# Kernel tuning notes

Hardware: AMD Instinct MI355X
Metric: run time of the kernel (lower is better)

Reference implementation:

```python
import jax, jax.numpy as jnp
import numpy as np

N, NFEAT, NFEAT_EXT, NHID, NCLASS, NHEADS = 8192, 512, 128, 256, 10, 8


def setup_inputs() -> dict:
    key = jax.random.key(0)
    ks = jax.random.split(key, 12)
    s = lambda fan_in: 1.0 / np.sqrt(fan_in)
    return {
        "x": jax.random.normal(ks[0], (N, NFEAT), jnp.float32),
        "adj": jax.random.uniform(ks[1], (N, N), jnp.float32) / N,  # row-stochastic-ish normalized adjacency
        "sub_fea": jax.random.normal(ks[2], (1, NFEAT_EXT), jnp.float32),
        # GraphConvolution 1: nfeat -> nhid
        "gc1_W": jax.random.normal(ks[3], (NFEAT, NHID), jnp.float32) * s(NFEAT),
        "gc1_b": jnp.zeros((NHID,), jnp.float32),
        # GraphConvolution 2: nhid -> 2*nhid
        "gc2_W": jax.random.normal(ks[4], (NHID, 2 * NHID), jnp.float32) * s(NHID),
        "gc2_b": jnp.zeros((2 * NHID,), jnp.float32),
        # fc1: nfeat_ext -> nhid
        "fc1_W": jax.random.normal(ks[5], (NFEAT_EXT, NHID), jnp.float32) * s(NFEAT_EXT),
        "fc1_b": jnp.zeros((NHID,), jnp.float32),
        # AttentionLayer(3*nhid, nclass, nheads): per-head projection + softmax head gating
        "att_W": jax.random.normal(ks[6], (NHEADS, 3 * NHID, NCLASS), jnp.float32) * s(3 * NHID),
        "att_a": jax.random.normal(ks[7], (NHEADS, 3 * NHID), jnp.float32) * s(3 * NHID),
        "att_b": jnp.zeros((NCLASS,), jnp.float32),
    }


def reference(x, adj, sub_fea, gc1_W, gc1_b, gc2_W, gc2_b, fc1_W, fc1_b, att_W, att_a, att_b):
    # GCN layer 1: adj @ (x @ W) + b, then ReLU
    h = jax.nn.relu(adj @ (x @ gc1_W) + gc1_b)            # [N, nhid]
    # GCN layer 2
    h = jax.nn.relu(adj @ (h @ gc2_W) + gc2_b)            # [N, 2*nhid]
    # global_mean_pool(batch=None): mean over all nodes -> single graph vector
    g = jax.nn.selu(jnp.mean(h, axis=0, keepdims=True))    # [1, 2*nhid]
    # dropout is identity in eval mode
    x_ext = sub_fea @ fc1_W + fc1_b                        # [1, nhid]
    z = jnp.concatenate([g, x_ext], axis=1)                # [1, 3*nhid]
    # multi-head attention fusion: softmax over head scores gating per-head projections
    scores = jnp.einsum("bi,hi->bh", z, att_a)            # [1, nheads]
    alpha = jax.nn.softmax(scores, axis=1)
    head_out = jnp.einsum("bi,hio->bho", z, att_W)        # [1, nheads, nclass]
    out = jnp.einsum("bh,bho->bo", alpha, head_out) + att_b  # [1, nclass]
    return jax.nn.log_softmax(out, axis=1)
```

## Files before the change

kernel.cpp:

```cpp
#include <hip/hip_runtime.h>

typedef __attribute__((ext_vector_type(8))) short short8;
typedef __attribute__((ext_vector_type(4))) float floatx4;
typedef unsigned short ushort_t;
typedef unsigned int u32;

__device__ __forceinline__ ushort_t f2bf(float x) {
  union { float f; unsigned int u; } v; v.f = x;
  unsigned int u = v.u;
  return (ushort_t)((u + 0x7FFFu + ((u >> 16) & 1u)) >> 16);
}
__device__ __forceinline__ unsigned int pk2(float a, float b) {
  return (unsigned int)f2bf(a) | ((unsigned int)f2bf(b) << 16);
}
__device__ __forceinline__ void gl_lds16(const void* g, void* l) {
  __builtin_amdgcn_global_load_lds(
      (const __attribute__((address_space(1))) u32*)g,
      (__attribute__((address_space(3))) u32*)l, 16, 0, 0);
}


__global__ void prep_t(const float* __restrict__ W1, const float* __restrict__ W2,
                       ushort_t* __restrict__ W1T, ushort_t* __restrict__ W2T) {
  int idx = blockIdx.x * 256 + threadIdx.x;
  int m = idx >> 9, k = idx & 511;
  W1T[((m >> 7) * 64 + (k >> 3)) * 1024 + (m & 127) * 8 + (k & 7)] = f2bf(W1[k * 256 + m]);
  int m2 = idx >> 8, k2 = idx & 255;
  W2T[((m2 >> 7) * 32 + (k2 >> 3)) * 1024 + (m2 & 127) * 8 + (k2 & 7)] = f2bf(W2[k2 * 512 + m2]);
}

__global__ __launch_bounds__(256) void tile_cvt(const float* __restrict__ src,
                                                ushort_t* __restrict__ dst, const int K) {
  __shared__ __align__(16) ushort_t ls[33024];
  const int t = threadIdx.x;
  const int rb = blockIdx.y, cb = blockIdx.x;
  const long sbase = (long)rb * 128 * K + cb * 256;
#pragma unroll 4
  for (int i = 0; i < 32; ++i) {
    int flat = i * 256 + t;
    int row = flat >> 6, kq = flat & 63;
    float4 v = *(const float4*)(src + sbase + (long)row * K + kq * 4);
    *(uint2*)(ls + ((kq >> 1) * 129 + row) * 8 + (kq & 1) * 4) =
        make_uint2(pk2(v.x, v.y), pk2(v.z, v.w));
  }
  __syncthreads();
  ushort_t* ob = dst + ((long)rb * (K >> 3) + cb * 32) * 1024;
  const uint4* lv = (const uint4*)ls;
  uint4* ov = (uint4*)ob;
#pragma unroll 4
  for (int i = 0; i < 16; ++i) {
    int o = i * 256 + t;
    ov[o] = lv[(o >> 7) * 129 + (o & 127)];
  }
}

template<int MT, int NT, int EPI>
__global__ __launch_bounds__(256, 2)
void gemm_t(const ushort_t* __restrict__ A, const ushort_t* __restrict__ B,
            const float* __restrict__ bias, float* __restrict__ Cf,
            float* __restrict__ gacc, const int K, const int N) {
  constexpr int MF = MT / 32, NF = NT / 32;
  constexpr int nA = MT / 64, nB = NT / 64;
  __shared__ __align__(16) ushort_t Als[MT * 32];
  __shared__ __align__(16) ushort_t Bls[NT * 32];

  const int t = threadIdx.x;
  const int lane = t & 63, w = t >> 6;
  const int wm = w >> 1, wn = w & 1;
  const int ml = lane & 15, quad = lane >> 4;
  const int m0 = blockIdx.y * MT, n0 = blockIdx.x * NT;
  const int Kper = K / gridDim.z, kbeg = blockIdx.z * Kper;

  const char* Ag = (const char*)(A + ((long)((m0 / MT) * (K >> 3) + (kbeg >> 3)) * MT) * 8);
  const char* Bg = (const char*)(B + ((long)((n0 / NT) * (K >> 3) + (kbeg >> 3)) * NT) * 8);

  floatx4 acc[MF][NF] = {};
  const int iters = Kper >> 5;
  for (int it = 0; it < iters; ++it) {
    __syncthreads();
#pragma unroll
    for (int c = 0; c < nA; ++c)
      gl_lds16(Ag + c * 4096 + t * 16, (char*)Als + c * 4096 + t * 16);
#pragma unroll
    for (int c = 0; c < nB; ++c)
      gl_lds16(Bg + c * 4096 + t * 16, (char*)Bls + c * 4096 + t * 16);
    Ag += MT * 64; Bg += NT * 64;
    __syncthreads();

    short8 av[MF], bv[NF];
#pragma unroll
    for (int f = 0; f < MF; ++f)
      av[f] = *(const short8*)(Als + (quad * MT + wm * (MT / 2) + f * 16 + ml) * 8);
#pragma unroll
    for (int f = 0; f < NF; ++f)
      bv[f] = *(const short8*)(Bls + (quad * NT + wn * (NT / 2) + f * 16 + ml) * 8);
#pragma unroll
    for (int fm = 0; fm < MF; ++fm)
#pragma unroll
      for (int fn = 0; fn < NF; ++fn)
        acc[fm][fn] = __builtin_amdgcn_mfma_f32_16x16x32_bf16(av[fm], bv[fn], acc[fm][fn], 0, 0, 0);
  }

  if constexpr (EPI == 2) {
#pragma unroll
    for (int fm = 0; fm < MF; ++fm) {
      int rowb = m0 + wm * (MT / 2) + fm * 16 + quad * 4;
#pragma unroll
      for (int r = 0; r < 4; ++r) {
        float bb = bias[rowb + r];
        float s = 0.f;
#pragma unroll
        for (int fn = 0; fn < NF; ++fn)
          s += fmaxf(acc[fm][fn][r] + bb, 0.f);
        s += __shfl_xor(s, 1);
        s += __shfl_xor(s, 2);
        s += __shfl_xor(s, 4);
        s += __shfl_xor(s, 8);
        if (ml == 0) atomicAdd(gacc + rowb + r, s);
      }
    }
  } else if constexpr (EPI == 3) {
    const int tv = (NT == 256) ? blockIdx.y : blockIdx.x;
    float* base = Cf + ((long)blockIdx.z * 64 + tv) * 32768 + (w * MF * NF * 4) * 64 + lane;
#pragma unroll
    for (int fm = 0; fm < MF; ++fm)
#pragma unroll
      for (int fn = 0; fn < NF; ++fn)
#pragma unroll
        for (int r = 0; r < 4; ++r)
          base[((fm * NF + fn) * 4 + r) * 64] = acc[fm][fn][r];
  } else {
    ushort_t* C = (ushort_t*)Cf;
#pragma unroll
    for (int fm = 0; fm < MF; ++fm)
#pragma unroll
      for (int fn = 0; fn < NF; ++fn) {
        int gm = m0 + wm * (MT / 2) + fm * 16 + quad * 4;
        int gn = n0 + wn * (NT / 2) + fn * 16 + ml;
        long ob = (long)(gn >> 3) * 2048 + (gn & 7);
#pragma unroll
        for (int r = 0; r < 4; ++r)
          C[ob + (long)(gm + r) * 8] = f2bf(acc[fm][fn][r]);
      }
  }
}

__global__ void reduce_L1b(const float* __restrict__ p, ushort_t* __restrict__ h1T,
                           const float* __restrict__ bias) {
  long i = (long)blockIdx.x * 256 + threadIdx.x;
  long o = i * 4;
  int j0 = (int)(o & 7);
  int row = (int)((o >> 3) & 255);
  int kc = (int)(o >> 11);
  int k0 = kc * 8 + j0;
  int tx = k0 >> 7, c0 = k0 & 127;
  int wm = row >> 7, fm = (row >> 4) & 7, quad = (row >> 2) & 3, r = row & 3;
  int wn = c0 >> 6, fn = (c0 >> 4) & 3, ml = c0 & 15;
  int slot = ((((wm * 2 + wn) * 8 + fm) * 4 + fn) * 4 + r) * 64 + quad * 16 + ml;
  const float* src = p + (long)tx * 32768 + slot;
  float4 s = *(const float4*)src;
  for (int z = 1; z < 8; ++z) {
    float4 b = *(const float4*)(src + (long)z * 2097152);
    s.x += b.x; s.y += b.y; s.z += b.z; s.w += b.w;
  }
  float bb = bias[row];
  s.x = fmaxf(s.x + bb, 0.f); s.y = fmaxf(s.y + bb, 0.f);
  s.z = fmaxf(s.z + bb, 0.f); s.w = fmaxf(s.w + bb, 0.f);
  *(uint2*)(h1T + o) = make_uint2(pk2(s.x, s.y), pk2(s.z, s.w));
}

__global__ void reduce_L2a(const float* __restrict__ p, ushort_t* __restrict__ P_t) {
  long i = (long)blockIdx.x * 256 + threadIdx.x;
  long o = i * 4;
  int j0 = (int)(o & 7);
  int row = (int)((o >> 3) & 127);
  int kc = (int)((o >> 10) & 31);
  int ty = (int)(o >> 15);
  int k0 = kc * 8 + j0;
  int wm = row >> 6, fm = (row >> 4) & 3, quad = (row >> 2) & 3, r = row & 3;
  int wn = k0 >> 7, fn = (k0 >> 4) & 7, ml = k0 & 15;
  int slot = ((((wm * 2 + wn) * 4 + fm) * 8 + fn) * 4 + r) * 64 + quad * 16 + ml;
  const float* src = p + (long)ty * 32768 + slot;
  float4 s = *(const float4*)src;
  for (int z = 1; z < 8; ++z) {
    float4 b = *(const float4*)(src + (long)z * 2097152);
    s.x += b.x; s.y += b.y; s.z += b.z; s.w += b.w;
  }
  *(uint2*)(P_t + o) = make_uint2(pk2(s.x, s.y), pk2(s.z, s.w));
}

__global__ void tail_kernel(const float* __restrict__ gacc, const float* __restrict__ sub_fea,
                            const float* __restrict__ fc1_W, const float* __restrict__ fc1_b,
                            const float* __restrict__ att_W, const float* __restrict__ att_a,
                            const float* __restrict__ att_b, float* __restrict__ out) {
  __shared__ float z[768];
  __shared__ float sc[8];
  __shared__ float alpha[8];
  __shared__ float outsh[10];
  const int t = threadIdx.x;

  for (int j = t; j < 512; j += 256) {
    float x = gacc[j] * (1.0f / 8192.0f);
    const float scale = 1.0507009873554805f, al = 1.6732632423543772f;
    z[j] = x > 0.f ? scale * x : scale * al * (expf(x) - 1.0f);
  }
  {
    float a = fc1_b[t];
    for (int i = 0; i < 128; ++i) a += sub_fea[i] * fc1_W[i * 256 + t];
    z[512 + t] = a;
  }
  if (t < 10) outsh[t] = 0.f;
  __syncthreads();

  {
    int h = t >> 5, ln = t & 31;
    float p = 0.f;
    for (int i = ln; i < 768; i += 32) p += z[i] * att_a[h * 768 + i];
    for (int m = 16; m; m >>= 1) p += __shfl_down(p, m, 32);
    if (ln == 0) sc[h] = p;
  }
  __syncthreads();
  if (t == 0) {
    float mx = sc[0];
    for (int h = 1; h < 8; ++h) mx = fmaxf(mx, sc[h]);
    float s = 0.f, e[8];
    for (int h = 0; h < 8; ++h) { e[h] = expf(sc[h] - mx); s += e[h]; }
    for (int h = 0; h < 8; ++h) alpha[h] = e[h] / s;
  }
  __syncthreads();

  float p[10];
#pragma unroll
  for (int o = 0; o < 10; ++o) p[o] = 0.f;
  for (int i = t; i < 768; i += 256) {
    float zi = z[i];
    for (int h = 0; h < 8; ++h) {
      float za = zi * alpha[h];
      const float* wp = att_W + (h * 768 + i) * 10;
#pragma unroll
      for (int o = 0; o < 10; ++o) p[o] += za * wp[o];
    }
  }
#pragma unroll
  for (int o = 0; o < 10; ++o) atomicAdd(&outsh[o], p[o]);
  __syncthreads();
  if (t == 0) {
    float v[10], mx = -1e30f;
    for (int o = 0; o < 10; ++o) { v[o] = outsh[o] + att_b[o]; mx = fmaxf(mx, v[o]); }
    float s = 0.f;
    for (int o = 0; o < 10; ++o) s += expf(v[o] - mx);
    float lse = logf(s) + mx;
    for (int o = 0; o < 10; ++o) out[o] = v[o] - lse;
  }
}

extern "C" void kernel_launch(void* const* d_in, const int* in_sizes, int n_in,
                              void* d_out, int out_size, void* d_ws, size_t ws_size,
                              hipStream_t stream) {
  const float* x       = (const float*)d_in[0];
  const float* adj     = (const float*)d_in[1];
  const float* sub_fea = (const float*)d_in[2];
  const float* gc1_W   = (const float*)d_in[3];
  const float* gc1_b   = (const float*)d_in[4];
  const float* gc2_W   = (const float*)d_in[5];
  const float* gc2_b   = (const float*)d_in[6];
  const float* fc1_W   = (const float*)d_in[7];
  const float* fc1_b   = (const float*)d_in[8];
  const float* att_W   = (const float*)d_in[9];
  const float* att_a   = (const float*)d_in[10];
  const float* att_b   = (const float*)d_in[11];
  float* out = (float*)d_out;

  const size_t MB = 1u << 20;
  char* ws = (char*)d_ws;
  size_t off = 0;
  ushort_t* adjT = (ushort_t*)(ws + off); off += 128 * MB;
  ushort_t* xT   = (ushort_t*)(ws + off); off += 8 * MB;
  ushort_t* t1T  = (ushort_t*)(ws + off); off += 4 * MB;
  ushort_t* h1T  = (ushort_t*)(ws + off); off += 4 * MB;
  ushort_t* P_t  = (ushort_t*)(ws + off); off += 4 * MB;
  float*    part = (float*)   (ws + off); off += 64 * MB;
  ushort_t* W1T  = (ushort_t*)(ws + off); off += 262144;
  ushort_t* W2T  = (ushort_t*)(ws + off); off += 262144;
  float*    gacc = (float*)   (ws + off);

  hipMemsetAsync(gacc, 0, 512 * sizeof(float), stream);
  prep_t<<<512, 256, 0, stream>>>(gc1_W, gc2_W, W1T, W2T);

  tile_cvt<<<dim3(32, 64), 256, 0, stream>>>(adj, adjT, 8192);
  tile_cvt<<<dim3(2, 64), 256, 0, stream>>>(x, xT, 512);

  gemm_t<128, 128, 4><<<dim3(64, 2, 1), 256, 0, stream>>>(
      W1T, xT, nullptr, (float*)t1T, nullptr, 512, 8192);

  gemm_t<256, 128, 3><<<dim3(64, 1, 8), 256, 0, stream>>>(
      t1T, adjT, nullptr, part, nullptr, 8192, 8192);
  reduce_L1b<<<2048, 256, 0, stream>>>(part, h1T, gc1_b);

  gemm_t<128, 256, 3><<<dim3(1, 64, 8), 256, 0, stream>>>(
      adjT, h1T, nullptr, part, nullptr, 8192, 256);
  reduce_L2a<<<2048, 256, 0, stream>>>(part, P_t);

  gemm_t<128, 128, 2><<<dim3(64, 4, 1), 256, 0, stream>>>(
      W2T, P_t, gc2_b, nullptr, gacc, 256, 8192);

  tail_kernel<<<1, 256, 0, stream>>>(gacc, sub_fea, fc1_W, fc1_b, att_W, att_a, att_b, out);
}
```

Measured before the change: 644.3 us.

## Double-buffer GEMM LDS tiles and store split-K partials as bf16

The GEMM main loop now uses two LDS buffers and issues the global-to-LDS loads for the next K-slice before computing on the current one, with one barrier per iteration instead of two. This is meant to overlap load latency with MFMA work, at the cost of doubled shared memory, which may reduce occupancy. Split-K partial results are also packed to bf16 pairs instead of fp32, halving the partial buffer's write and read traffic in the reduce kernels. The trade is some accuracy loss, since eight bf16-rounded partials are summed.

```diff
diff --git a/kernel.cpp b/kernel.cpp
--- a/kernel.cpp
+++ b/kernel.cpp
@@ -12,6 +12,12 @@
 }
 __device__ __forceinline__ unsigned int pk2(float a, float b) {
   return (unsigned int)f2bf(a) | ((unsigned int)f2bf(b) << 16);
+}
+__device__ __forceinline__ float bf_lo(u32 u) {
+  union { u32 u; float f; } v; v.u = u << 16; return v.f;
+}
+__device__ __forceinline__ float bf_hi(u32 u) {
+  union { u32 u; float f; } v; v.u = u & 0xFFFF0000u; return v.f;
 }
 __device__ __forceinline__ void gl_lds16(const void* g, void* l) {
   __builtin_amdgcn_global_load_lds(
@@ -61,8 +67,8 @@
             float* __restrict__ gacc, const int K, const int N) {
   constexpr int MF = MT / 32, NF = NT / 32;
   constexpr int nA = MT / 64, nB = NT / 64;
-  __shared__ __align__(16) ushort_t Als[MT * 32];
-  __shared__ __align__(16) ushort_t Bls[NT * 32];
+  __shared__ __align__(16) ushort_t Als[2][MT * 32];
+  __shared__ __align__(16) ushort_t Bls[2][NT * 32];
 
   const int t = threadIdx.x;
   const int lane = t & 63, w = t >> 6;
@@ -76,24 +82,35 @@
 
   floatx4 acc[MF][NF] = {};
   const int iters = Kper >> 5;
+
+#pragma unroll
+  for (int c = 0; c < nA; ++c)
+    gl_lds16(Ag + c * 4096 + t * 16, (char*)Als[0] + c * 4096 + t * 16);
+#pragma unroll
+  for (int c = 0; c < nB; ++c)
+    gl_lds16(Bg + c * 4096 + t * 16, (char*)Bls[0] + c * 4096 + t * 16);
+  Ag += MT * 64; Bg += NT * 64;
+
   for (int it = 0; it < iters; ++it) {
+    const int cur = it & 1, nxt = cur ^ 1;
     __syncthreads();
-#pragma unroll
-    for (int c = 0; c < nA; ++c)
-      gl_lds16(Ag + c * 4096 + t * 16, (char*)Als + c * 4096 + t * 16);
-#pragma unroll
-    for (int c = 0; c < nB; ++c)
-      gl_lds16(Bg + c * 4096 + t * 16, (char*)Bls + c * 4096 + t * 16);
-    Ag += MT * 64; Bg += NT * 64;
-    __syncthreads();
+    if (it + 1 < iters) {
+#pragma unroll
+      for (int c = 0; c < nA; ++c)
+        gl_lds16(Ag + c * 4096 + t * 16, (char*)Als[nxt] + c * 4096 + t * 16);
+#pragma unroll
+      for (int c = 0; c < nB; ++c)
+        gl_lds16(Bg + c * 4096 + t * 16, (char*)Bls[nxt] + c * 4096 + t * 16);
+      Ag += MT * 64; Bg += NT * 64;
+    }
 
     short8 av[MF], bv[NF];
 #pragma unroll
     for (int f = 0; f < MF; ++f)
-      av[f] = *(const short8*)(Als + (quad * MT + wm * (MT / 2) + f * 16 + ml) * 8);
+      av[f] = *(const short8*)(&Als[cur][0] + (quad * MT + wm * (MT / 2) + f * 16 + ml) * 8);
 #pragma unroll
     for (int f = 0; f < NF; ++f)
-      bv[f] = *(const short8*)(Bls + (quad * NT + wn * (NT / 2) + f * 16 + ml) * 8);
+      bv[f] = *(const short8*)(&Bls[cur][0] + (quad * NT + wn * (NT / 2) + f * 16 + ml) * 8);
 #pragma unroll
     for (int fm = 0; fm < MF; ++fm)
 #pragma unroll
@@ -121,14 +138,16 @@
     }
   } else if constexpr (EPI == 3) {
     const int tv = (NT == 256) ? blockIdx.y : blockIdx.x;
-    float* base = Cf + ((long)blockIdx.z * 64 + tv) * 32768 + (w * MF * NF * 4) * 64 + lane;
+    u32* base = (u32*)Cf + ((long)blockIdx.z * 64 + tv) * (MF * NF * 8 * 64)
+                + (w * MF * NF * 2) * 64 + lane;
 #pragma unroll
     for (int fm = 0; fm < MF; ++fm)
 #pragma unroll
       for (int fn = 0; fn < NF; ++fn)
 #pragma unroll
-        for (int r = 0; r < 4; ++r)
-          base[((fm * NF + fn) * 4 + r) * 64] = acc[fm][fn][r];
+        for (int rp = 0; rp < 2; ++rp)
+          base[((fm * NF + fn) * 2 + rp) * 64] =
+              pk2(acc[fm][fn][2 * rp], acc[fm][fn][2 * rp + 1]);
   } else {
     ushort_t* C = (ushort_t*)Cf;
 #pragma unroll
@@ -145,48 +164,49 @@
   }
 }
 
-__global__ void reduce_L1b(const float* __restrict__ p, ushort_t* __restrict__ h1T,
+__global__ void reduce_L1b(const u32* __restrict__ p, ushort_t* __restrict__ h1T,
                            const float* __restrict__ bias) {
   long i = (long)blockIdx.x * 256 + threadIdx.x;
   long o = i * 4;
-  int j0 = (int)(o & 7);
   int row = (int)((o >> 3) & 255);
-  int kc = (int)(o >> 11);
-  int k0 = kc * 8 + j0;
+  int k0 = (int)((o >> 11) << 3) + (int)(o & 7);
   int tx = k0 >> 7, c0 = k0 & 127;
   int wm = row >> 7, fm = (row >> 4) & 7, quad = (row >> 2) & 3, r = row & 3;
   int wn = c0 >> 6, fn = (c0 >> 4) & 3, ml = c0 & 15;
-  int slot = ((((wm * 2 + wn) * 8 + fm) * 4 + fn) * 4 + r) * 64 + quad * 16 + ml;
-  const float* src = p + (long)tx * 32768 + slot;
-  float4 s = *(const float4*)src;
-  for (int z = 1; z < 8; ++z) {
-    float4 b = *(const float4*)(src + (long)z * 2097152);
-    s.x += b.x; s.y += b.y; s.z += b.z; s.w += b.w;
+  int slot = (((wm * 2 + wn) * 8 + fm) * 4 + fn) * 2 + (r >> 1);
+  const u32* src = p + (long)tx * 16384 + slot * 64 + quad * 16 + ml;
+  const bool hi = r & 1;
+  float s0 = 0, s1 = 0, s2 = 0, s3 = 0;
+  for (int z = 0; z < 8; ++z) {
+    uint4 v = *(const uint4*)(src + (long)z * 1048576);
+    if (hi) { s0 += bf_hi(v.x); s1 += bf_hi(v.y); s2 += bf_hi(v.z); s3 += bf_hi(v.w); }
+    else    { s0 += bf_lo(v.x); s1 += bf_lo(v.y); s2 += bf_lo(v.z); s3 += bf_lo(v.w); }
   }
   float bb = bias[row];
-  s.x = fmaxf(s.x + bb, 0.f); s.y = fmaxf(s.y + bb, 0.f);
-  s.z = fmaxf(s.z + bb, 0.f); s.w = fmaxf(s.w + bb, 0.f);
-  *(uint2*)(h1T + o) = make_uint2(pk2(s.x, s.y), pk2(s.z, s.w));
-}
-
-__global__ void reduce_L2a(const float* __restrict__ p, ushort_t* __restrict__ P_t) {
+  s0 = fmaxf(s0 + bb, 0.f); s1 = fmaxf(s1 + bb, 0.f);
+  s2 = fmaxf(s2 + bb, 0.f); s3 = fmaxf(s3 + bb, 0.f);
+  *(uint2*)(h1T + o) = make_uint2(pk2(s0, s1), pk2(s2, s3));
+}
+
+__global__ void reduce_L2a(const u32* __restrict__ p, ushort_t* __restrict__ P_t) {
   long i = (long)blockIdx.x * 256 + threadIdx.x;
   long o = i * 4;
-  int j0 = (int)(o & 7);
   int row = (int)((o >> 3) & 127);
   int kc = (int)((o >> 10) & 31);
   int ty = (int)(o >> 15);
-  int k0 = kc * 8 + j0;
+  int k0 = kc * 8 + (int)(o & 7);
   int wm = row >> 6, fm = (row >> 4) & 3, quad = (row >> 2) & 3, r = row & 3;
   int wn = k0 >> 7, fn = (k0 >> 4) & 7, ml = k0 & 15;
-  int slot = ((((wm * 2 + wn) * 4 + fm) * 8 + fn) * 4 + r) * 64 + quad * 16 + ml;
-  const float* src = p + (long)ty * 32768 + slot;
-  float4 s = *(const float4*)src;
-  for (int z = 1; z < 8; ++z) {
-    float4 b = *(const float4*)(src + (long)z * 2097152);
-    s.x += b.x; s.y += b.y; s.z += b.z; s.w += b.w;
-  }
-  *(uint2*)(P_t + o) = make_uint2(pk2(s.x, s.y), pk2(s.z, s.w));
+  int slot = (((wm * 2 + wn) * 4 + fm) * 8 + fn) * 2 + (r >> 1);
+  const u32* src = p + (long)ty * 16384 + slot * 64 + quad * 16 + ml;
+  const bool hi = r & 1;
+  float s0 = 0, s1 = 0, s2 = 0, s3 = 0;
+  for (int z = 0; z < 8; ++z) {
+    uint4 v = *(const uint4*)(src + (long)z * 1048576);
+    if (hi) { s0 += bf_hi(v.x); s1 += bf_hi(v.y); s2 += bf_hi(v.z); s3 += bf_hi(v.w); }
+    else    { s0 += bf_lo(v.x); s1 += bf_lo(v.y); s2 += bf_lo(v.z); s3 += bf_lo(v.w); }
+  }
+  *(uint2*)(P_t + o) = make_uint2(pk2(s0, s1), pk2(s2, s3));
 }
 
 __global__ void tail_kernel(const float* __restrict__ gacc, const float* __restrict__ sub_fea,
@@ -279,7 +299,7 @@
   ushort_t* t1T  = (ushort_t*)(ws + off); off += 4 * MB;
   ushort_t* h1T  = (ushort_t*)(ws + off); off += 4 * MB;
   ushort_t* P_t  = (ushort_t*)(ws + off); off += 4 * MB;
-  float*    part = (float*)   (ws + off); off += 64 * MB;
+  u32*      part = (u32*)     (ws + off); off += 32 * MB;
   ushort_t* W1T  = (ushort_t*)(ws + off); off += 262144;
   ushort_t* W2T  = (ushort_t*)(ws + off); off += 262144;
   float*    gacc = (float*)   (ws + off);
@@ -294,11 +314,11 @@
       W1T, xT, nullptr, (float*)t1T, nullptr, 512, 8192);
 
   gemm_t<256, 128, 3><<<dim3(64, 1, 8), 256, 0, stream>>>(
-      t1T, adjT, nullptr, part, nullptr, 8192, 8192);
+      t1T, adjT, nullptr, (float*)part, nullptr, 8192, 8192);
   reduce_L1b<<<2048, 256, 0, stream>>>(part, h1T, gc1_b);
 
   gemm_t<128, 256, 3><<<dim3(1, 64, 8), 256, 0, stream>>>(
-      adjT, h1T, nullptr, part, nullptr, 8192, 256);
+      adjT, h1T, nullptr, (float*)part, nullptr, 8192, 256);
   reduce_L2a<<<2048, 256, 0, stream>>>(part, P_t);
 
   gemm_t<128, 128, 2><<<dim3(64, 4, 1), 256, 0, stream>>>(
```

Measured after the change: 615.6 us. -4.4%, faster.
